# Optimization experiments

Hardware: AMD Instinct MI355X
Metric: run time of the kernel (lower is better)

## Reference

```python
import jax, jax.numpy as jnp
import numpy as np

TAIL = 10.0
K = 8
MIN_W = 1e-3
MIN_H = 1e-3
MIN_D = 1e-3
EPS = 1e-12
D_ID = 32   # identity dims
D_TR = 32   # transformed dims
HID = 256


def setup_inputs() -> dict:
    key = jax.random.key(0)
    k0, k1, k2, k3, k4 = jax.random.split(key, 5)
    B = 131072
    inputs = jax.random.normal(k0, (B, D_ID + D_TR), dtype=jnp.float32)
    W1 = jax.random.normal(k1, (D_ID, HID), dtype=jnp.float32) * (1.0 / np.sqrt(D_ID))
    b1 = jnp.zeros((HID,), dtype=jnp.float32)
    W2 = jax.random.normal(k2, (HID, D_TR * (3 * K + 1)), dtype=jnp.float32) * (1.0 / np.sqrt(HID))
    b2 = jnp.zeros((D_TR * (3 * K + 1),), dtype=jnp.float32)
    return {"inputs": inputs, "W1": W1, "b1": b1, "W2": W2, "b2": b2}


def _normalize_bin_params(un_w, un_h, un_d):
    # widths
    w = jax.nn.softmax(un_w, axis=-1)
    w = MIN_W + (1.0 - MIN_W * K) * w
    cw = jnp.cumsum(w, axis=-1)
    cw = jnp.pad(cw, [(0, 0)] * (cw.ndim - 1) + [(1, 0)])
    cw = cw / jnp.clip(cw[..., -1:], 1e-12)
    w = cw[..., 1:] - cw[..., :-1]
    # heights
    h = jax.nn.softmax(un_h, axis=-1)
    h = MIN_H + (1.0 - MIN_H * K) * h
    ch = jnp.cumsum(h, axis=-1)
    ch = jnp.pad(ch, [(0, 0)] * (ch.ndim - 1) + [(1, 0)])
    ch = ch / jnp.clip(ch[..., -1:], 1e-12)
    h = ch[..., 1:] - ch[..., :-1]
    d = MIN_D + jax.nn.softplus(un_d)
    return w, cw, h, ch, d


def _rqs_forward(x, w, cw, h, ch, d):
    # x: (N,); bins: (N,K) / (N,K+1). Linear tails outside [-TAIL, TAIL].
    inside = (x >= -TAIL) & (x <= TAIL)
    xs = jnp.clip((x + TAIL) / (2.0 * TAIL), 0.0, 1.0)
    bin_ids = jnp.clip(jnp.sum(xs[:, None] >= cw, axis=-1) - 1, 0, K - 1)
    take = lambda t, idx: jnp.take_along_axis(t, idx[:, None], axis=-1)[:, 0]
    xk = take(cw, bin_ids)
    wk = take(w, bin_ids)
    yk = take(ch, bin_ids)
    hk = take(h, bin_ids)
    dk = take(d, bin_ids)
    dk1 = take(d, bin_ids + 1)
    t = jnp.clip((xs - xk) / (wk + EPS), 0.0, 1.0)
    a = (hk + EPS) / (wk + EPS)
    b = dk
    c = dk1
    num = a * t * t + b * t * (1.0 - t)
    den = a + (b + c - 2.0 * a) * t * (1.0 - t)
    s = num / (den + EPS)
    ys = yk + hk * s
    y = ys * (2.0 * TAIL) - TAIL
    deriv_num = a * a * (c * t * t + 2.0 * a * t * (1.0 - t) + b * (1.0 - t) * (1.0 - t))
    dydx = deriv_num / (den * den + EPS)  # (top-bottom)/(right-left) == 1
    lad = jnp.log(jnp.clip(dydx, 1e-12))
    return jnp.where(inside, y, x), jnp.where(inside, lad, 0.0)


def reference(inputs, W1, b1, W2, b2):
    identity = inputs[:, :D_ID]          # mask <= 0 columns
    to_transform = inputs[:, D_ID:]      # mask > 0 columns
    Bsz = inputs.shape[0]
    params = jax.nn.relu(identity @ W1 + b1) @ W2 + b2
    p = params.reshape(Bsz, D_TR, 3 * K + 1)
    un_w, un_h, un_d = p[..., :K], p[..., K:2 * K], p[..., 2 * K:]
    w, cw, h, ch, d = _normalize_bin_params(un_w, un_h, un_d)
    # flatten (Bsz, D_TR, ...) -> (Bsz*D_TR, ...)
    xf = to_transform.reshape(-1)
    yf, ladf = _rqs_forward(
        xf,
        w.reshape(-1, K), cw.reshape(-1, K + 1),
        h.reshape(-1, K), ch.reshape(-1, K + 1),
        d.reshape(-1, K + 1),
    )
    outputs = jnp.concatenate([identity, yf.reshape(Bsz, D_TR)], axis=1)
    logabsdet = ladf.reshape(Bsz, D_TR).sum(axis=1)
    return outputs, logabsdet
```

## Files before the change

kernel.cpp:

```cpp
#include <hip/hip_runtime.h>
#include <math.h>

#define NROWS 131072
#define HID 256
#define NPAR 800
#define MROWS 32
#define NTHREADS 512
#define NBLOCKS (NROWS / MROWS)

#define W2F_FRAGS 25600
#define W1F_BASE  51200
#define LDS_HLO 16384
#define LDS_X   32768
#define LDS_PLD 804
#define LDS_TOTAL (16 * LDS_PLD * 4)

typedef __attribute__((ext_vector_type(8))) short s16x8;
typedef __attribute__((ext_vector_type(4))) float f32x4;

__device__ __forceinline__ unsigned short bf16_rne(float f) {
    unsigned u = __float_as_uint(f);
    u += 0x7fffu + ((u >> 16) & 1u);
    return (unsigned short)(u >> 16);
}
__device__ __forceinline__ float bf16_to_f(unsigned short h) {
    return __uint_as_float((unsigned)h << 16);
}

__global__ void prep_w(const float* __restrict__ W2, const float* __restrict__ W1,
                       short* __restrict__ wsp)
{
    const int t = blockIdx.x * 256 + threadIdx.x;
    if (t < W2F_FRAGS) {
        const int l = t & 63;
        const int g = t >> 6;
        const int ct = g >> 3, k0 = g & 7;
        const int c  = (ct << 4) + (l & 15);
        const int kb = (k0 << 5) + ((l >> 4) << 3);
        s16x8 hi, lo;
#pragma unroll
        for (int j = 0; j < 8; ++j) {
            float v = W2[(size_t)(kb + j) * NPAR + c];
            unsigned short h = bf16_rne(v);
            unsigned short lw = bf16_rne(v - bf16_to_f(h));
            hi[j] = (short)h;
            lo[j] = (short)lw;
        }
        ((s16x8*)wsp)[g * 128 + l * 2]     = hi;
        ((s16x8*)wsp)[g * 128 + l * 2 + 1] = lo;
    } else if (t < W2F_FRAGS + 1024) {
        const int t1 = t - W2F_FRAGS;
        const int l  = t1 & 63;
        const int ct = t1 >> 6;
        const int c  = (ct << 4) + (l & 15);
        const int kb = (l >> 4) << 3;
        s16x8 hi, lo;
#pragma unroll
        for (int j = 0; j < 8; ++j) {
            float v = W1[(size_t)(kb + j) * HID + c];
            unsigned short h = bf16_rne(v);
            unsigned short lw = bf16_rne(v - bf16_to_f(h));
            hi[j] = (short)h;
            lo[j] = (short)lw;
        }
        ((s16x8*)wsp)[W1F_BASE + ct * 128 + l * 2]     = hi;
        ((s16x8*)wsp)[W1F_BASE + ct * 128 + l * 2 + 1] = lo;
    }
}

__global__ __launch_bounds__(NTHREADS, 4)
void rqs_fused(const float* __restrict__ inp,
               const float* __restrict__ b1,
               const short* __restrict__ W2F,
               const float* __restrict__ b2,
               float* __restrict__ out)
{
    extern __shared__ char smem[];
    char*  hhi   = smem;
    char*  hlo   = smem + LDS_HLO;
    char*  x_c   = smem + LDS_X;
    float* p_lds = (float*)smem;

    const int t    = threadIdx.x;
    const int row0 = blockIdx.x * MROWS;
    const int lane = t & 63;
    const int w    = t >> 6;
    const int arow = lane & 15;
    const int kgrp = lane >> 4;
    const int lane2 = lane << 1;

    const s16x8* BF = (const s16x8*)W2F;

    const int nct = (w < 2) ? 7 : 6;

    if (t < 256) {
        const int r = t >> 3, q = t & 7;
        const float4 v = ((const float4*)(inp + (size_t)(row0 + r) * 64))[q];
        ((float4*)(out + (size_t)(row0 + r) * 64))[q] = v;
        int byte = (r << 7) + (q << 4);
        byte ^= (r & 7) << 4;
        *(float4*)(x_c + byte) = v;
    }
    __syncthreads();

    {
        const int c0 = (2 * w) * 128 + W1F_BASE + lane2;
        const int c1 = (2 * w + 1) * 128 + W1F_BASE + lane2;
        const s16x8 w1h0 = BF[c0], w1l0 = BF[c0 + 1];
        const s16x8 w1h1 = BF[c1], w1l1 = BF[c1 + 1];

        s16x8 xhi[2], xlo[2];
#pragma unroll
        for (int rt = 0; rt < 2; ++rt) {
            const int row  = rt * 16 + arow;
            const int base = (row << 7) + (kgrp << 5);
            const int sw   = (row & 7) << 4;
            const float4 va = *(const float4*)(x_c + (base ^ sw));
            const float4 vb = *(const float4*)(x_c + ((base + 16) ^ sw));
            const float xv[8] = {va.x, va.y, va.z, va.w, vb.x, vb.y, vb.z, vb.w};
#pragma unroll
            for (int j = 0; j < 8; ++j) {
                unsigned short h = bf16_rne(xv[j]);
                xhi[rt][j] = (short)h;
                xlo[rt][j] = (short)bf16_rne(xv[j] - bf16_to_f(h));
            }
        }

        const float bias0 = b1[(2 * w) * 16 + arow];
        const float bias1 = b1[(2 * w + 1) * 16 + arow];
        f32x4 g[2][2];
        g[0][0] = (f32x4){bias0, bias0, bias0, bias0};
        g[1][0] = (f32x4){bias0, bias0, bias0, bias0};
        g[0][1] = (f32x4){bias1, bias1, bias1, bias1};
        g[1][1] = (f32x4){bias1, bias1, bias1, bias1};

#pragma unroll
        for (int rt = 0; rt < 2; ++rt) {
            g[rt][0] = __builtin_amdgcn_mfma_f32_16x16x32_bf16(xhi[rt], w1h0, g[rt][0], 0, 0, 0);
            g[rt][1] = __builtin_amdgcn_mfma_f32_16x16x32_bf16(xhi[rt], w1h1, g[rt][1], 0, 0, 0);
            g[rt][0] = __builtin_amdgcn_mfma_f32_16x16x32_bf16(xhi[rt], w1l0, g[rt][0], 0, 0, 0);
            g[rt][1] = __builtin_amdgcn_mfma_f32_16x16x32_bf16(xhi[rt], w1l1, g[rt][1], 0, 0, 0);
            g[rt][0] = __builtin_amdgcn_mfma_f32_16x16x32_bf16(xlo[rt], w1h0, g[rt][0], 0, 0, 0);
            g[rt][1] = __builtin_amdgcn_mfma_f32_16x16x32_bf16(xlo[rt], w1h1, g[rt][1], 0, 0, 0);
        }

#pragma unroll
        for (int rt = 0; rt < 2; ++rt) {
#pragma unroll
            for (int ci = 0; ci < 2; ++ci) {
                const int col = (2 * w + ci) * 16 + arow;
#pragma unroll
                for (int i = 0; i < 4; ++i) {
                    const int row = rt * 16 + (kgrp << 2) + i;
                    const float s = fmaxf(g[rt][ci][i], 0.0f);
                    unsigned short hs = bf16_rne(s);
                    unsigned short ls = bf16_rne(s - bf16_to_f(hs));
                    int byte = (row << 9) + (col << 1);
                    byte ^= (row & 7) << 4;
                    *(short*)(hhi + byte) = (short)hs;
                    *(short*)(hlo + byte) = (short)ls;
                }
            }
        }
    }
    __syncthreads();

    f32x4 acc[7][2];
#pragma unroll
    for (int ci = 0; ci < 7; ++ci) {
        acc[ci][0] = (f32x4){0.f, 0.f, 0.f, 0.f};
        acc[ci][1] = (f32x4){0.f, 0.f, 0.f, 0.f};
    }

#pragma unroll 1
    for (int k0 = 0; k0 < 8; ++k0) {
        s16x8 ahi[2], alo[2];
#pragma unroll
        for (int rt = 0; rt < 2; ++rt) {
            const int row = rt * 16 + arow;
            int byte = (row << 9) + (k0 << 6) + (kgrp << 4);
            byte ^= (row & 7) << 4;
            ahi[rt] = *(const s16x8*)(hhi + byte);
            alo[rt] = *(const s16x8*)(hlo + byte);
        }
#pragma unroll
        for (int ci = 0; ci < 7; ++ci) {
            if (ci < nct) {
                const int ct = w + (ci << 3);
                const int f  = (ct * 8 + k0) * 128 + lane2;
                const s16x8 bh = BF[f];
                const s16x8 bl = BF[f + 1];
                __builtin_amdgcn_s_setprio(1);
                acc[ci][0] = __builtin_amdgcn_mfma_f32_16x16x32_bf16(ahi[0], bh, acc[ci][0], 0, 0, 0);
                acc[ci][1] = __builtin_amdgcn_mfma_f32_16x16x32_bf16(ahi[1], bh, acc[ci][1], 0, 0, 0);
                acc[ci][0] = __builtin_amdgcn_mfma_f32_16x16x32_bf16(ahi[0], bl, acc[ci][0], 0, 0, 0);
                acc[ci][1] = __builtin_amdgcn_mfma_f32_16x16x32_bf16(ahi[1], bl, acc[ci][1], 0, 0, 0);
                acc[ci][0] = __builtin_amdgcn_mfma_f32_16x16x32_bf16(alo[0], bh, acc[ci][0], 0, 0, 0);
                acc[ci][1] = __builtin_amdgcn_mfma_f32_16x16x32_bf16(alo[1], bh, acc[ci][1], 0, 0, 0);
                __builtin_amdgcn_s_setprio(0);
            }
        }
    }

#pragma unroll
    for (int rhalf = 0; rhalf < 2; ++rhalf) {
        __syncthreads();
#pragma unroll
        for (int ci = 0; ci < 7; ++ci) {
            if (ci < nct) {
                const int ct = w + (ci << 3);
                const float bias = b2[(ct << 4) + arow];
                const int col = (ct << 4) + arow;
                const f32x4 v = acc[ci][rhalf];
                const int rowl = kgrp << 2;
                p_lds[(rowl + 0) * LDS_PLD + col] = v[0] + bias;
                p_lds[(rowl + 1) * LDS_PLD + col] = v[1] + bias;
                p_lds[(rowl + 2) * LDS_PLD + col] = v[2] + bias;
                p_lds[(rowl + 3) * LDS_PLD + col] = v[3] + bias;
            }
        }
        __syncthreads();

        {
            const int r_l = t >> 5;
            const int dl  = t & 31;
            const float* p = &p_lds[r_l * LDS_PLD + dl * 25];
            float pv[25];
#pragma unroll
            for (int j = 0; j < 25; ++j) pv[j] = p[j];

            float cw[9], ch[9];
            {
                float mw = pv[0];
#pragma unroll
                for (int j = 1; j < 8; ++j) mw = fmaxf(mw, pv[j]);
                float e[8], sw = 0.f;
#pragma unroll
                for (int j = 0; j < 8; ++j) { e[j] = __expf(pv[j] - mw); sw += e[j]; }
                const float scale = 0.992f / sw;
                float run = 0.f;
                cw[0] = 0.f;
#pragma unroll
                for (int j = 0; j < 8; ++j) { run += 0.001f + e[j] * scale; cw[j + 1] = run; }
                const float icn = 1.0f / fmaxf(cw[8], 1e-12f);
#pragma unroll
                for (int j = 1; j <= 8; ++j) cw[j] *= icn;
            }
            {
                float mh = pv[8];
#pragma unroll
                for (int j = 1; j < 8; ++j) mh = fmaxf(mh, pv[8 + j]);
                float e[8], sh = 0.f;
#pragma unroll
                for (int j = 0; j < 8; ++j) { e[j] = __expf(pv[8 + j] - mh); sh += e[j]; }
                const float scale = 0.992f / sh;
                float run = 0.f;
                ch[0] = 0.f;
#pragma unroll
                for (int j = 0; j < 8; ++j) { run += 0.001f + e[j] * scale; ch[j + 1] = run; }
                const float icn = 1.0f / fmaxf(ch[8], 1e-12f);
#pragma unroll
                for (int j = 1; j <= 8; ++j) ch[j] *= icn;
            }

            const int grow = row0 + rhalf * 16 + r_l;
            const float x = inp[(size_t)grow * 64 + 32 + dl];
            const float xs = fminf(fmaxf((x + 10.0f) * 0.05f, 0.f), 1.f);
            int b = 0;
#pragma unroll
            for (int j = 1; j <= 8; ++j) b += (xs >= cw[j]) ? 1 : 0;
            b = min(b, 7);

            float xk = 0.f, wk = 0.f, yk = 0.f, hk = 0.f;
#pragma unroll
            for (int j = 0; j < 8; ++j) {
                if (b == j) {
                    xk = cw[j]; wk = cw[j + 1] - cw[j];
                    yk = ch[j]; hk = ch[j + 1] - ch[j];
                }
            }
            float ud0 = pv[16], ud1 = pv[17];
#pragma unroll
            for (int j = 1; j < 8; ++j) {
                const bool ge = (b >= j);
                ud0 = ge ? pv[16 + j] : ud0;
                ud1 = ge ? pv[17 + j] : ud1;
            }
            const float dk  = 0.001f + fmaxf(ud0, 0.f) + __logf(1.0f + __expf(-fabsf(ud0)));
            const float dk1 = 0.001f + fmaxf(ud1, 0.f) + __logf(1.0f + __expf(-fabsf(ud1)));

            const float EPSf = 1e-12f;
            const float tt = fminf(fmaxf((xs - xk) / (wk + EPSf), 0.f), 1.f);
            const float a = (hk + EPSf) / (wk + EPSf);
            const float omt = 1.f - tt;
            const float tomt = tt * omt;
            const float num = a * tt * tt + dk * tomt;
            const float den = a + (dk + dk1 - 2.f * a) * tomt;
            const float sres = num / (den + EPSf);
            const float ys = yk + hk * sres;
            float y = ys * 20.0f - 10.0f;
            const float dnum = a * a * (dk1 * tt * tt + 2.f * a * tomt + dk * omt * omt);
            const float dydx = dnum / (den * den + EPSf);
            float lad = __logf(fmaxf(dydx, 1e-12f));

            const bool inside = (x >= -10.0f) && (x <= 10.0f);
            if (!inside) { y = x; lad = 0.0f; }

            out[(size_t)grow * 64 + 32 + dl] = y;

            float s = lad;
            s += __shfl_xor(s, 1, 64);
            s += __shfl_xor(s, 2, 64);
            s += __shfl_xor(s, 4, 64);
            s += __shfl_xor(s, 8, 64);
            s += __shfl_xor(s, 16, 64);
            if ((lane & 31) == 0) out[(size_t)NROWS * 64 + grow] = s;
        }
    }
}

extern "C" void kernel_launch(void* const* d_in, const int* in_sizes, int n_in,
                              void* d_out, int out_size, void* d_ws, size_t ws_size,
                              hipStream_t stream) {
    const float* inp = (const float*)d_in[0];
    const float* W1  = (const float*)d_in[1];
    const float* b1  = (const float*)d_in[2];
    const float* W2  = (const float*)d_in[3];
    const float* b2  = (const float*)d_in[4];
    float* out = (float*)d_out;
    short* wsp = (short*)d_ws;

    hipLaunchKernelGGL(prep_w, dim3(104), dim3(256), 0, stream, W2, W1, wsp);
    hipLaunchKernelGGL(rqs_fused, dim3(NBLOCKS), dim3(NTHREADS), LDS_TOTAL, stream,
                       inp, b1, (const short*)wsp, b2, out);
}
```

Baseline: 268.5 us.

## Halve block to 256 threads, give each wave more column tiles and rows

```diff
diff --git a/kernel.cpp b/kernel.cpp
--- a/kernel.cpp
+++ b/kernel.cpp
@@ -5,7 +5,7 @@
 #define HID 256
 #define NPAR 800
 #define MROWS 32
-#define NTHREADS 512
+#define NTHREADS 256
 #define NBLOCKS (NROWS / MROWS)
 
 #define W2F_FRAGS 25600
@@ -68,7 +68,7 @@
     }
 }
 
-__global__ __launch_bounds__(NTHREADS, 4)
+__global__ __launch_bounds__(NTHREADS, 3)
 void rqs_fused(const float* __restrict__ inp,
                const float* __restrict__ b1,
                const short* __restrict__ W2F,
@@ -91,9 +91,9 @@
 
     const s16x8* BF = (const s16x8*)W2F;
 
-    const int nct = (w < 2) ? 7 : 6;
-
-    if (t < 256) {
+    const int nct = (w < 2) ? 13 : 12;
+
+    {
         const int r = t >> 3, q = t & 7;
         const float4 v = ((const float4*)(inp + (size_t)(row0 + r) * 64))[q];
         ((float4*)(out + (size_t)(row0 + r) * 64))[q] = v;
@@ -104,10 +104,13 @@
     __syncthreads();
 
     {
-        const int c0 = (2 * w) * 128 + W1F_BASE + lane2;
-        const int c1 = (2 * w + 1) * 128 + W1F_BASE + lane2;
-        const s16x8 w1h0 = BF[c0], w1l0 = BF[c0 + 1];
-        const s16x8 w1h1 = BF[c1], w1l1 = BF[c1 + 1];
+        s16x8 w1h[4], w1l[4];
+#pragma unroll
+        for (int cc = 0; cc < 4; ++cc) {
+            const int f = (4 * w + cc) * 128 + W1F_BASE + lane2;
+            w1h[cc] = BF[f];
+            w1l[cc] = BF[f + 1];
+        }
 
         s16x8 xhi[2], xlo[2];
 #pragma unroll
@@ -126,33 +129,33 @@
             }
         }
 
-        const float bias0 = b1[(2 * w) * 16 + arow];
-        const float bias1 = b1[(2 * w + 1) * 16 + arow];
-        f32x4 g[2][2];
-        g[0][0] = (f32x4){bias0, bias0, bias0, bias0};
-        g[1][0] = (f32x4){bias0, bias0, bias0, bias0};
-        g[0][1] = (f32x4){bias1, bias1, bias1, bias1};
-        g[1][1] = (f32x4){bias1, bias1, bias1, bias1};
+        f32x4 g[2][4];
+#pragma unroll
+        for (int cc = 0; cc < 4; ++cc) {
+            const float bias = b1[(4 * w + cc) * 16 + arow];
+            g[0][cc] = (f32x4){bias, bias, bias, bias};
+            g[1][cc] = (f32x4){bias, bias, bias, bias};
+        }
 
 #pragma unroll
         for (int rt = 0; rt < 2; ++rt) {
-            g[rt][0] = __builtin_amdgcn_mfma_f32_16x16x32_bf16(xhi[rt], w1h0, g[rt][0], 0, 0, 0);
-            g[rt][1] = __builtin_amdgcn_mfma_f32_16x16x32_bf16(xhi[rt], w1h1, g[rt][1], 0, 0, 0);
-            g[rt][0] = __builtin_amdgcn_mfma_f32_16x16x32_bf16(xhi[rt], w1l0, g[rt][0], 0, 0, 0);
-            g[rt][1] = __builtin_amdgcn_mfma_f32_16x16x32_bf16(xhi[rt], w1l1, g[rt][1], 0, 0, 0);
-            g[rt][0] = __builtin_amdgcn_mfma_f32_16x16x32_bf16(xlo[rt], w1h0, g[rt][0], 0, 0, 0);
-            g[rt][1] = __builtin_amdgcn_mfma_f32_16x16x32_bf16(xlo[rt], w1h1, g[rt][1], 0, 0, 0);
+#pragma unroll
+            for (int cc = 0; cc < 4; ++cc) {
+                g[rt][cc] = __builtin_amdgcn_mfma_f32_16x16x32_bf16(xhi[rt], w1h[cc], g[rt][cc], 0, 0, 0);
+                g[rt][cc] = __builtin_amdgcn_mfma_f32_16x16x32_bf16(xhi[rt], w1l[cc], g[rt][cc], 0, 0, 0);
+                g[rt][cc] = __builtin_amdgcn_mfma_f32_16x16x32_bf16(xlo[rt], w1h[cc], g[rt][cc], 0, 0, 0);
+            }
         }
 
 #pragma unroll
         for (int rt = 0; rt < 2; ++rt) {
 #pragma unroll
-            for (int ci = 0; ci < 2; ++ci) {
-                const int col = (2 * w + ci) * 16 + arow;
+            for (int cc = 0; cc < 4; ++cc) {
+                const int col = (4 * w + cc) * 16 + arow;
 #pragma unroll
                 for (int i = 0; i < 4; ++i) {
                     const int row = rt * 16 + (kgrp << 2) + i;
-                    const float s = fmaxf(g[rt][ci][i], 0.0f);
+                    const float s = fmaxf(g[rt][cc][i], 0.0f);
                     unsigned short hs = bf16_rne(s);
                     unsigned short ls = bf16_rne(s - bf16_to_f(hs));
                     int byte = (row << 9) + (col << 1);
@@ -165,9 +168,9 @@
     }
     __syncthreads();
 
-    f32x4 acc[7][2];
-#pragma unroll
-    for (int ci = 0; ci < 7; ++ci) {
+    f32x4 acc[13][2];
+#pragma unroll
+    for (int ci = 0; ci < 13; ++ci) {
         acc[ci][0] = (f32x4){0.f, 0.f, 0.f, 0.f};
         acc[ci][1] = (f32x4){0.f, 0.f, 0.f, 0.f};
     }
@@ -184,9 +187,9 @@
             alo[rt] = *(const s16x8*)(hlo + byte);
         }
 #pragma unroll
-        for (int ci = 0; ci < 7; ++ci) {
+        for (int ci = 0; ci < 13; ++ci) {
             if (ci < nct) {
-                const int ct = w + (ci << 3);
+                const int ct = w + (ci << 2);
                 const int f  = (ct * 8 + k0) * 128 + lane2;
                 const s16x8 bh = BF[f];
                 const s16x8 bl = BF[f + 1];
@@ -206,9 +209,9 @@
     for (int rhalf = 0; rhalf < 2; ++rhalf) {
         __syncthreads();
 #pragma unroll
-        for (int ci = 0; ci < 7; ++ci) {
+        for (int ci = 0; ci < 13; ++ci) {
             if (ci < nct) {
-                const int ct = w + (ci << 3);
+                const int ct = w + (ci << 2);
                 const float bias = b2[(ct << 4) + arow];
                 const int col = (ct << 4) + arow;
                 const f32x4 v = acc[ci][rhalf];
@@ -222,99 +225,116 @@
         __syncthreads();
 
         {
-            const int r_l = t >> 5;
             const int dl  = t & 31;
-            const float* p = &p_lds[r_l * LDS_PLD + dl * 25];
-            float pv[25];
-#pragma unroll
-            for (int j = 0; j < 25; ++j) pv[j] = p[j];
-
-            float cw[9], ch[9];
-            {
-                float mw = pv[0];
-#pragma unroll
-                for (int j = 1; j < 8; ++j) mw = fmaxf(mw, pv[j]);
+            const int r_b = t >> 5;
+
+            float pv[2][25];
+#pragma unroll
+            for (int u = 0; u < 2; ++u) {
+                const float* p = &p_lds[(r_b + 8 * u) * LDS_PLD + dl * 25];
+#pragma unroll
+                for (int j = 0; j < 25; ++j) pv[u][j] = p[j];
+            }
+
+            float cw[2][9], chh[2][9];
+#pragma unroll
+            for (int u = 0; u < 2; ++u) {
+                float mw = pv[u][0];
+#pragma unroll
+                for (int j = 1; j < 8; ++j) mw = fmaxf(mw, pv[u][j]);
                 float e[8], sw = 0.f;
 #pragma unroll
-                for (int j = 0; j < 8; ++j) { e[j] = __expf(pv[j] - mw); sw += e[j]; }
+                for (int j = 0; j < 8; ++j) { e[j] = __expf(pv[u][j] - mw); sw += e[j]; }
                 const float scale = 0.992f / sw;
                 float run = 0.f;
-                cw[0] = 0.f;
-#pragma unroll
-                for (int j = 0; j < 8; ++j) { run += 0.001f + e[j] * scale; cw[j + 1] = run; }
-                const float icn = 1.0f / fmaxf(cw[8], 1e-12f);
-#pragma unroll
-                for (int j = 1; j <= 8; ++j) cw[j] *= icn;
-            }
-            {
-                float mh = pv[8];
-#pragma unroll
-                for (int j = 1; j < 8; ++j) mh = fmaxf(mh, pv[8 + j]);
+                cw[u][0] = 0.f;
+#pragma unroll
+                for (int j = 0; j < 8; ++j) { run += 0.001f + e[j] * scale; cw[u][j + 1] = run; }
+                const float icn = 1.0f / fmaxf(cw[u][8], 1e-12f);
+#pragma unroll
+                for (int j = 1; j <= 8; ++j) cw[u][j] *= icn;
+            }
+#pragma unroll
+            for (int u = 0; u < 2; ++u) {
+                float mh = pv[u][8];
+#pragma unroll
+                for (int j = 1; j < 8; ++j) mh = fmaxf(mh, pv[u][8 + j]);
                 float e[8], sh = 0.f;
 #pragma unroll
-                for (int j = 0; j < 8; ++j) { e[j] = __expf(pv[8 + j] - mh); sh += e[j]; }
+                for (int j = 0; j < 8; ++j) { e[j] = __expf(pv[u][8 + j] - mh); sh += e[j]; }
                 const float scale = 0.992f / sh;
                 float run = 0.f;
-                ch[0] = 0.f;
-#pragma unroll
-                for (int j = 0; j < 8; ++j) { run += 0.001f + e[j] * scale; ch[j + 1] = run; }
-                const float icn = 1.0f / fmaxf(ch[8], 1e-12f);
-#pragma unroll
-                for (int j = 1; j <= 8; ++j) ch[j] *= icn;
-            }
-
-            const int grow = row0 + rhalf * 16 + r_l;
-            const float x = inp[(size_t)grow * 64 + 32 + dl];
-            const float xs = fminf(fmaxf((x + 10.0f) * 0.05f, 0.f), 1.f);
-            int b = 0;
-#pragma unroll
-            for (int j = 1; j <= 8; ++j) b += (xs >= cw[j]) ? 1 : 0;
-            b = min(b, 7);
-
-            float xk = 0.f, wk = 0.f, yk = 0.f, hk = 0.f;
-#pragma unroll
-            for (int j = 0; j < 8; ++j) {
-                if (b == j) {
-                    xk = cw[j]; wk = cw[j + 1] - cw[j];
-                    yk = ch[j]; hk = ch[j + 1] - ch[j];
+                chh[u][0] = 0.f;
+#pragma unroll
+                for (int j = 0; j < 8; ++j) { run += 0.001f + e[j] * scale; chh[u][j + 1] = run; }
+                const float icn = 1.0f / fmaxf(chh[u][8], 1e-12f);
+#pragma unroll
+                for (int j = 1; j <= 8; ++j) chh[u][j] *= icn;
+            }
+
+            float lad[2], yv[2], xin[2];
+#pragma unroll
+            for (int u = 0; u < 2; ++u) {
+                const int grow = row0 + rhalf * 16 + r_b + 8 * u;
+                const float x = inp[(size_t)grow * 64 + 32 + dl];
+                xin[u] = x;
+                const float xs = fminf(fmaxf((x + 10.0f) * 0.05f, 0.f), 1.f);
+                int b = 0;
+#pragma unroll
+                for (int j = 1; j <= 8; ++j) b += (xs >= cw[u][j]) ? 1 : 0;
+                b = min(b, 7);
+
+                float xk = 0.f, wk = 0.f, yk = 0.f, hk = 0.f;
+#pragma unroll
+                for (int j = 0; j < 8; ++j) {
+                    if (b == j) {
+                        xk = cw[u][j]; wk = cw[u][j + 1] - cw[u][j];
+                        yk = chh[u][j]; hk = chh[u][j + 1] - chh[u][j];
+                    }
                 }
-            }
-            float ud0 = pv[16], ud1 = pv[17];
-#pragma unroll
-            for (int j = 1; j < 8; ++j) {
-                const bool ge = (b >= j);
-                ud0 = ge ? pv[16 + j] : ud0;
-                ud1 = ge ? pv[17 + j] : ud1;
-            }
-            const float dk  = 0.001f + fmaxf(ud0, 0.f) + __logf(1.0f + __expf(-fabsf(ud0)));
-            const float dk1 = 0.001f + fmaxf(ud1, 0.f) + __logf(1.0f + __expf(-fabsf(ud1)));
-
-            const float EPSf = 1e-12f;
-            const float tt = fminf(fmaxf((xs - xk) / (wk + EPSf), 0.f), 1.f);
-            const float a = (hk + EPSf) / (wk + EPSf);
-            const float omt = 1.f - tt;
-            const float tomt = tt * omt;
-            const float num = a * tt * tt + dk * tomt;
-            const float den = a + (dk + dk1 - 2.f * a) * tomt;
-            const float sres = num / (den + EPSf);
-            const float ys = yk + hk * sres;
-            float y = ys * 20.0f - 10.0f;
-            const float dnum = a * a * (dk1 * tt * tt + 2.f * a * tomt + dk * omt * omt);
-            const float dydx = dnum / (den * den + EPSf);
-            float lad = __logf(fmaxf(dydx, 1e-12f));
-
-            const bool inside = (x >= -10.0f) && (x <= 10.0f);
-            if (!inside) { y = x; lad = 0.0f; }
-
-            out[(size_t)grow * 64 + 32 + dl] = y;
-
-            float s = lad;
-            s += __shfl_xor(s, 1, 64);
-            s += __shfl_xor(s, 2, 64);
-            s += __shfl_xor(s, 4, 64);
-            s += __shfl_xor(s, 8, 64);
-            s += __shfl_xor(s, 16, 64);
-            if ((lane & 31) == 0) out[(size_t)NROWS * 64 + grow] = s;
+                float ud0 = pv[u][16], ud1 = pv[u][17];
+#pragma unroll
+                for (int j = 1; j < 8; ++j) {
+                    const bool ge = (b >= j);
+                    ud0 = ge ? pv[u][16 + j] : ud0;
+                    ud1 = ge ? pv[u][17 + j] : ud1;
+                }
+                const float dk  = 0.001f + fmaxf(ud0, 0.f) + __logf(1.0f + __expf(-fabsf(ud0)));
+                const float dk1 = 0.001f + fmaxf(ud1, 0.f) + __logf(1.0f + __expf(-fabsf(ud1)));
+
+                const float EPSf = 1e-12f;
+                const float tt = fminf(fmaxf((xs - xk) / (wk + EPSf), 0.f), 1.f);
+                const float a = (hk + EPSf) / (wk + EPSf);
+                const float omt = 1.f - tt;
+                const float tomt = tt * omt;
+                const float num = a * tt * tt + dk * tomt;
+                const float den = a + (dk + dk1 - 2.f * a) * tomt;
+                const float sres = num / (den + EPSf);
+                const float ys = yk + hk * sres;
+                float y = ys * 20.0f - 10.0f;
+                const float dnum = a * a * (dk1 * tt * tt + 2.f * a * tomt + dk * omt * omt);
+                const float dydx = dnum / (den * den + EPSf);
+                float l = __logf(fmaxf(dydx, 1e-12f));
+
+                const bool inside = (x >= -10.0f) && (x <= 10.0f);
+                if (!inside) { y = x; l = 0.0f; }
+                yv[u] = y;
+                lad[u] = l;
+            }
+
+#pragma unroll
+            for (int u = 0; u < 2; ++u) {
+                const int grow = row0 + rhalf * 16 + r_b + 8 * u;
+                out[(size_t)grow * 64 + 32 + dl] = yv[u];
+                float s = lad[u];
+                s += __shfl_xor(s, 1, 64);
+                s += __shfl_xor(s, 2, 64);
+                s += __shfl_xor(s, 4, 64);
+                s += __shfl_xor(s, 8, 64);
+                s += __shfl_xor(s, 16, 64);
+                if ((lane & 31) == 0) out[(size_t)NROWS * 64 + grow] = s;
+            }
+            (void)xin;
         }
     }
 }
```

New measurement: 276.9 us. +3.2%, slower.

## Double rows per block to 64 with 1024 threads to reuse W2 fragments

Applied to the files above, without the earlier changes.

```diff
diff --git a/kernel.cpp b/kernel.cpp
--- a/kernel.cpp
+++ b/kernel.cpp
@@ -4,16 +4,16 @@
 #define NROWS 131072
 #define HID 256
 #define NPAR 800
-#define MROWS 32
-#define NTHREADS 512
+#define MROWS 64
+#define NTHREADS 1024
 #define NBLOCKS (NROWS / MROWS)
 
 #define W2F_FRAGS 25600
 #define W1F_BASE  51200
-#define LDS_HLO 16384
-#define LDS_X   32768
+#define LDS_HLO 32768
+#define LDS_X   65536
 #define LDS_PLD 804
-#define LDS_TOTAL (16 * LDS_PLD * 4)
+#define LDS_TOTAL (32 * LDS_PLD * 4)
 
 typedef __attribute__((ext_vector_type(8))) short s16x8;
 typedef __attribute__((ext_vector_type(4))) float f32x4;
@@ -91,9 +91,9 @@
 
     const s16x8* BF = (const s16x8*)W2F;
 
-    const int nct = (w < 2) ? 7 : 6;
-
-    if (t < 256) {
+    const int nct = (w < 2) ? 4 : 3;
+
+    if (t < 512) {
         const int r = t >> 3, q = t & 7;
         const float4 v = ((const float4*)(inp + (size_t)(row0 + r) * 64))[q];
         ((float4*)(out + (size_t)(row0 + r) * 64))[q] = v;
@@ -104,14 +104,12 @@
     __syncthreads();
 
     {
-        const int c0 = (2 * w) * 128 + W1F_BASE + lane2;
-        const int c1 = (2 * w + 1) * 128 + W1F_BASE + lane2;
-        const s16x8 w1h0 = BF[c0], w1l0 = BF[c0 + 1];
-        const s16x8 w1h1 = BF[c1], w1l1 = BF[c1 + 1];
-
-        s16x8 xhi[2], xlo[2];
-#pragma unroll
-        for (int rt = 0; rt < 2; ++rt) {
+        const int f0 = w * 128 + W1F_BASE + lane2;
+        const s16x8 w1h = BF[f0], w1l = BF[f0 + 1];
+
+        s16x8 xhi[4], xlo[4];
+#pragma unroll
+        for (int rt = 0; rt < 4; ++rt) {
             const int row  = rt * 16 + arow;
             const int base = (row << 7) + (kgrp << 5);
             const int sw   = (row & 7) << 4;
@@ -126,57 +124,53 @@
             }
         }
 
-        const float bias0 = b1[(2 * w) * 16 + arow];
-        const float bias1 = b1[(2 * w + 1) * 16 + arow];
-        f32x4 g[2][2];
-        g[0][0] = (f32x4){bias0, bias0, bias0, bias0};
-        g[1][0] = (f32x4){bias0, bias0, bias0, bias0};
-        g[0][1] = (f32x4){bias1, bias1, bias1, bias1};
-        g[1][1] = (f32x4){bias1, bias1, bias1, bias1};
-
-#pragma unroll
-        for (int rt = 0; rt < 2; ++rt) {
-            g[rt][0] = __builtin_amdgcn_mfma_f32_16x16x32_bf16(xhi[rt], w1h0, g[rt][0], 0, 0, 0);
-            g[rt][1] = __builtin_amdgcn_mfma_f32_16x16x32_bf16(xhi[rt], w1h1, g[rt][1], 0, 0, 0);
-            g[rt][0] = __builtin_amdgcn_mfma_f32_16x16x32_bf16(xhi[rt], w1l0, g[rt][0], 0, 0, 0);
-            g[rt][1] = __builtin_amdgcn_mfma_f32_16x16x32_bf16(xhi[rt], w1l1, g[rt][1], 0, 0, 0);
-            g[rt][0] = __builtin_amdgcn_mfma_f32_16x16x32_bf16(xlo[rt], w1h0, g[rt][0], 0, 0, 0);
-            g[rt][1] = __builtin_amdgcn_mfma_f32_16x16x32_bf16(xlo[rt], w1h1, g[rt][1], 0, 0, 0);
-        }
-
-#pragma unroll
-        for (int rt = 0; rt < 2; ++rt) {
-#pragma unroll
-            for (int ci = 0; ci < 2; ++ci) {
-                const int col = (2 * w + ci) * 16 + arow;
-#pragma unroll
-                for (int i = 0; i < 4; ++i) {
-                    const int row = rt * 16 + (kgrp << 2) + i;
-                    const float s = fmaxf(g[rt][ci][i], 0.0f);
-                    unsigned short hs = bf16_rne(s);
-                    unsigned short ls = bf16_rne(s - bf16_to_f(hs));
-                    int byte = (row << 9) + (col << 1);
-                    byte ^= (row & 7) << 4;
-                    *(short*)(hhi + byte) = (short)hs;
-                    *(short*)(hlo + byte) = (short)ls;
-                }
+        const float bias = b1[w * 16 + arow];
+        f32x4 g[4];
+#pragma unroll
+        for (int rt = 0; rt < 4; ++rt) g[rt] = (f32x4){bias, bias, bias, bias};
+
+#pragma unroll
+        for (int rt = 0; rt < 4; ++rt) {
+            g[rt] = __builtin_amdgcn_mfma_f32_16x16x32_bf16(xhi[rt], w1h, g[rt], 0, 0, 0);
+            g[rt] = __builtin_amdgcn_mfma_f32_16x16x32_bf16(xhi[rt], w1l, g[rt], 0, 0, 0);
+            g[rt] = __builtin_amdgcn_mfma_f32_16x16x32_bf16(xlo[rt], w1h, g[rt], 0, 0, 0);
+        }
+
+#pragma unroll
+        for (int rt = 0; rt < 4; ++rt) {
+            const int col = w * 16 + arow;
+#pragma unroll
+            for (int i = 0; i < 4; ++i) {
+                const int row = rt * 16 + (kgrp << 2) + i;
+                const float s = fmaxf(g[rt][i], 0.0f);
+                unsigned short hs = bf16_rne(s);
+                unsigned short ls = bf16_rne(s - bf16_to_f(hs));
+                int byte = (row << 9) + (col << 1);
+                byte ^= (row & 7) << 4;
+                *(short*)(hhi + byte) = (short)hs;
+                *(short*)(hlo + byte) = (short)ls;
             }
         }
     }
     __syncthreads();
 
-    f32x4 acc[7][2];
-#pragma unroll
-    for (int ci = 0; ci < 7; ++ci) {
-        acc[ci][0] = (f32x4){0.f, 0.f, 0.f, 0.f};
-        acc[ci][1] = (f32x4){0.f, 0.f, 0.f, 0.f};
-    }
+    float x_ep[2];
+#pragma unroll
+    for (int ph = 0; ph < 2; ++ph)
+        x_ep[ph] = inp[(size_t)(row0 + ph * 32 + (t >> 5)) * 64 + 32 + (t & 31)];
+
+    f32x4 acc[4][4];
+#pragma unroll
+    for (int ci = 0; ci < 4; ++ci)
+#pragma unroll
+        for (int rt = 0; rt < 4; ++rt)
+            acc[ci][rt] = (f32x4){0.f, 0.f, 0.f, 0.f};
 
 #pragma unroll 1
     for (int k0 = 0; k0 < 8; ++k0) {
-        s16x8 ahi[2], alo[2];
-#pragma unroll
-        for (int rt = 0; rt < 2; ++rt) {
+        s16x8 ahi[4], alo[4];
+#pragma unroll
+        for (int rt = 0; rt < 4; ++rt) {
             const int row = rt * 16 + arow;
             int byte = (row << 9) + (k0 << 6) + (kgrp << 4);
             byte ^= (row & 7) << 4;
@@ -184,19 +178,19 @@
             alo[rt] = *(const s16x8*)(hlo + byte);
         }
 #pragma unroll
-        for (int ci = 0; ci < 7; ++ci) {
+        for (int ci = 0; ci < 4; ++ci) {
             if (ci < nct) {
-                const int ct = w + (ci << 3);
+                const int ct = w + (ci << 4);
                 const int f  = (ct * 8 + k0) * 128 + lane2;
                 const s16x8 bh = BF[f];
                 const s16x8 bl = BF[f + 1];
                 __builtin_amdgcn_s_setprio(1);
-                acc[ci][0] = __builtin_amdgcn_mfma_f32_16x16x32_bf16(ahi[0], bh, acc[ci][0], 0, 0, 0);
-                acc[ci][1] = __builtin_amdgcn_mfma_f32_16x16x32_bf16(ahi[1], bh, acc[ci][1], 0, 0, 0);
-                acc[ci][0] = __builtin_amdgcn_mfma_f32_16x16x32_bf16(ahi[0], bl, acc[ci][0], 0, 0, 0);
-                acc[ci][1] = __builtin_amdgcn_mfma_f32_16x16x32_bf16(ahi[1], bl, acc[ci][1], 0, 0, 0);
-                acc[ci][0] = __builtin_amdgcn_mfma_f32_16x16x32_bf16(alo[0], bh, acc[ci][0], 0, 0, 0);
-                acc[ci][1] = __builtin_amdgcn_mfma_f32_16x16x32_bf16(alo[1], bh, acc[ci][1], 0, 0, 0);
+#pragma unroll
+                for (int rt = 0; rt < 4; ++rt) {
+                    acc[ci][rt] = __builtin_amdgcn_mfma_f32_16x16x32_bf16(ahi[rt], bh, acc[ci][rt], 0, 0, 0);
+                    acc[ci][rt] = __builtin_amdgcn_mfma_f32_16x16x32_bf16(ahi[rt], bl, acc[ci][rt], 0, 0, 0);
+                    acc[ci][rt] = __builtin_amdgcn_mfma_f32_16x16x32_bf16(alo[rt], bh, acc[ci][rt], 0, 0, 0);
+                }
                 __builtin_amdgcn_s_setprio(0);
             }
         }
@@ -206,17 +200,21 @@
     for (int rhalf = 0; rhalf < 2; ++rhalf) {
         __syncthreads();
 #pragma unroll
-        for (int ci = 0; ci < 7; ++ci) {
+        for (int ci = 0; ci < 4; ++ci) {
             if (ci < nct) {
-                const int ct = w + (ci << 3);
+                const int ct = w + (ci << 4);
                 const float bias = b2[(ct << 4) + arow];
                 const int col = (ct << 4) + arow;
-                const f32x4 v = acc[ci][rhalf];
-                const int rowl = kgrp << 2;
-                p_lds[(rowl + 0) * LDS_PLD + col] = v[0] + bias;
-                p_lds[(rowl + 1) * LDS_PLD + col] = v[1] + bias;
-                p_lds[(rowl + 2) * LDS_PLD + col] = v[2] + bias;
-                p_lds[(rowl + 3) * LDS_PLD + col] = v[3] + bias;
+#pragma unroll
+                for (int rr = 0; rr < 2; ++rr) {
+                    const int rt = rhalf * 2 + rr;
+                    const f32x4 v = acc[ci][rt];
+                    const int rowl = (rr << 4) + (kgrp << 2);
+                    p_lds[(rowl + 0) * LDS_PLD + col] = v[0] + bias;
+                    p_lds[(rowl + 1) * LDS_PLD + col] = v[1] + bias;
+                    p_lds[(rowl + 2) * LDS_PLD + col] = v[2] + bias;
+                    p_lds[(rowl + 3) * LDS_PLD + col] = v[3] + bias;
+                }
             }
         }
         __syncthreads();
@@ -263,8 +261,8 @@
                 for (int j = 1; j <= 8; ++j) ch[j] *= icn;
             }
 
-            const int grow = row0 + rhalf * 16 + r_l;
-            const float x = inp[(size_t)grow * 64 + 32 + dl];
+            const int grow = row0 + rhalf * 32 + r_l;
+            const float x = x_ep[rhalf];
             const float xs = fminf(fmaxf((x + 10.0f) * 0.05f, 0.f), 1.f);
             int b = 0;
 #pragma unroll
@@ -330,6 +328,13 @@
     float* out = (float*)d_out;
     short* wsp = (short*)d_ws;
 
+    static bool attr_done = false;
+    if (!attr_done) {
+        hipFuncSetAttribute((const void*)rqs_fused,
+                            hipFuncAttributeMaxDynamicSharedMemorySize, LDS_TOTAL);
+        attr_done = true;
+    }
+
     hipLaunchKernelGGL(prep_w, dim3(104), dim3(256), 0, stream, W2, W1, wsp);
     hipLaunchKernelGGL(rqs_fused, dim3(NBLOCKS), dim3(NTHREADS), LDS_TOTAL, stream,
                        inp, b1, (const short*)wsp, b2, out);
```

New measurement: 268.5 us. About the same (+0.0%).
